# Kernel optimization log

Hardware: AMD Instinct MI355X
Metric: run time of the kernel (lower is better)

## Reference

```python
import jax, jax.numpy as jnp
import numpy as np

HID = 128
N_NODES = 50000
N_REL = 500
N_EDGES = 625000
BN_EPS = 1e-5
LRELU_SLOPE = 0.01


def _xavier(key, shape):
    fan_in, fan_out = shape[1], shape[0]
    std = float(np.sqrt(2.0 / (fan_in + fan_out)))
    return jax.random.normal(key, shape, dtype=jnp.float32) * std


def setup_inputs() -> dict:
    key = jax.random.key(0)
    ks = jax.random.split(key, 16)
    x = jax.random.normal(ks[0], (N_NODES, HID), dtype=jnp.float32)
    r = jax.random.normal(ks[1], (N_REL, HID), dtype=jnp.float32)
    que_context = jax.random.normal(ks[2], (1, HID), dtype=jnp.float32)
    fin_que = jax.random.normal(ks[3], (1, 1, HID), dtype=jnp.float32)
    edge_index = jax.random.randint(ks[4], (2, N_EDGES), 0, N_NODES, dtype=jnp.int64)
    edge_attr = jax.random.randint(ks[5], (N_EDGES,), 0, N_REL, dtype=jnp.int64)
    return {
        "x": x, "r": r, "que_context": que_context, "fin_que": fin_que,
        "edge_index": edge_index, "edge_attr": edge_attr,
        # mess_comp: Linear(2*hid, hid) + Tanh
        "W_mess": _xavier(ks[6], (HID, 2 * HID)), "b_mess": jnp.zeros((HID,), jnp.float32),
        # mess_atten_trans: Linear(2*hid, hid) + LeakyReLU
        "W_matt": _xavier(ks[7], (HID, 2 * HID)), "b_matt": jnp.zeros((HID,), jnp.float32),
        "mess_atten_weight": _xavier(ks[8], (1, HID)),
        # x_atten_trans: Linear(2*hid, hid) + LeakyReLU
        "W_xatt": _xavier(ks[9], (HID, 2 * HID)), "b_xatt": jnp.zeros((HID,), jnp.float32),
        "x_atten_weight": _xavier(ks[10], (1, HID)),
        # BatchNorm1d(hid) affine params (training-mode batch stats are used)
        "bn_gamma": jnp.ones((HID,), jnp.float32), "bn_beta": jnp.zeros((HID,), jnp.float32),
    }


def reference(x, r, que_context, fin_que, edge_index, edge_attr,
              W_mess, b_mess, W_matt, b_matt, mess_atten_weight,
              W_xatt, b_xatt, x_atten_weight, bn_gamma, bn_beta):
    n_nodes = x.shape[0]
    # BatchNorm1d over relation embeddings (training-mode: batch statistics, biased var)
    mu = jnp.mean(r, axis=0)
    var = jnp.mean(jnp.square(r - mu), axis=0)
    r = (r - mu) * jax.lax.rsqrt(var + BN_EPS) * bn_gamma + bn_beta

    head_ents, tail_ents = edge_index[0], edge_index[1]
    head_embeds = x[head_ents]            # [E, H]
    rel_embeds = r[edge_attr]             # [E, H]

    # message computation: Linear(2H->H) + tanh
    mess_in = jnp.concatenate([head_embeds, rel_embeds], axis=1)  # [E, 2H]
    mess = jnp.tanh(mess_in @ W_mess.T + b_mess)                  # [E, H]

    # message attention logits
    qc = jnp.broadcast_to(que_context, (mess.shape[0], que_context.shape[1]))
    mc = jnp.concatenate([mess, qc], axis=1) @ W_matt.T + b_matt
    mc = jax.nn.leaky_relu(mc, LRELU_SLOPE)
    mess_coeffs = jnp.sum(mess_atten_weight * mc, axis=1)         # [E]

    # segment softmax over tail_ents
    seg_max = jax.ops.segment_max(mess_coeffs, tail_ents, num_segments=n_nodes)
    mess_coeffs = jnp.exp(mess_coeffs - seg_max[tail_ents])
    seg_sum = jax.ops.segment_sum(mess_coeffs, tail_ents, num_segments=n_nodes)
    mess_weights = mess_coeffs / (seg_sum[tail_ents] + 1e-16)

    # weighted scatter-sum aggregation
    sum_mess = jax.ops.segment_sum(mess * mess_weights[:, None], tail_ents,
                                   num_segments=n_nodes)          # [N, H]

    # gating attention between x and aggregated messages
    pair = jnp.stack([x, sum_mess], axis=1)                       # [N, 2, H]
    fq = jnp.broadcast_to(fin_que, (n_nodes, 2, fin_que.shape[2]))
    xc = jnp.concatenate([pair, fq], axis=2)                      # [N, 2, 2H]
    xc = jax.nn.leaky_relu(jnp.einsum('nkc,hc->nkh', xc, W_xatt) + b_xatt, LRELU_SLOPE)
    x_coeffs = jnp.sum(x_atten_weight[None] * xc, axis=2)         # [N, 2]
    x_weight = jax.nn.softmax(x_coeffs, axis=1)
    x_out = x_weight[:, 0:1] * x + x_weight[:, 1:2] * sum_mess
    # dropout is identity (eval / p=0)
    return x_out, r
```

## Files before the change

### kernel.cpp

```cpp
#include <hip/hip_runtime.h>
#include <hip/hip_bf16.h>

#define HID 128
#define NN 50000
#define NR 500
#define NE 625000
#define LRELU 0.01f
#define SCAN_BLOCKS 196

typedef __hip_bfloat16 bf16;
typedef __attribute__((ext_vector_type(8))) short short8;
typedef __attribute__((ext_vector_type(4))) float float4_;

__device__ __forceinline__ float b2f(bf16 v) { return __bfloat162float(v); }
__device__ __forceinline__ bf16 f2b(float v) { return __float2bfloat16(v); }

__device__ __forceinline__ float san(float v) {
    return (v == v && v > -1e30f && v < 1e30f) ? v : 0.f;
}

__device__ __forceinline__ float ftanh(float a) {
    float e = __expf(2.f * a);
    return 1.f - 2.f * __builtin_amdgcn_rcpf(e + 1.f);
}

__device__ __forceinline__ float ldf(const void* p, int i, int f32) {
    return f32 ? ((const float*)p)[i] : b2f(((const bf16*)p)[i]);
}
__device__ __forceinline__ void stf(void* p, int i, float v, int f32) {
    if (f32) ((float*)p)[i] = v;
    else ((bf16*)p)[i] = f2b(v);
}

__device__ __forceinline__ int clampi(int v, int hi) {
    return v < 0 ? 0 : (v >= hi ? hi - 1 : v);
}
__device__ __forceinline__ int idx_at(const int* p, int i, int is64) {
    return p[is64 ? (2 * i) : i];
}

__device__ __forceinline__ unsigned short bfbits(float v) {
    bf16 h = f2b(v);
    return *(unsigned short*)&h;
}
__device__ __forceinline__ unsigned int packbf2(float a, float b) {
    return (unsigned int)bfbits(a) | ((unsigned int)bfbits(b) << 16);
}
__device__ __forceinline__ float bflo(unsigned int u) { return __uint_as_float(u << 16); }
__device__ __forceinline__ float bfhi(unsigned int u) { return __uint_as_float(u & 0xffff0000u); }

__device__ __forceinline__ float xorReduce16(float v) {
    v += __shfl_xor(v, 1, 64);
    v += __shfl_xor(v, 2, 64);
    v += __shfl_xor(v, 4, 64);
    v += __shfl_xor(v, 8, 64);
    return v;
}
__device__ __forceinline__ float waveMax(float v) {
#pragma unroll
    for (int o = 1; o < 64; o <<= 1) v = fmaxf(v, __shfl_xor(v, o, 64));
    return v;
}
__device__ __forceinline__ float waveSum(float v) {
#pragma unroll
    for (int o = 1; o < 64; o <<= 1) v += __shfl_xor(v, o, 64);
    return v;
}

struct DetectArr {
    const void* p[16];
    int sz[16];
    int kind[16];
};

__global__ void detect_all(DetectArr d, int* __restrict__ flags) {
    int b = blockIdx.x;
    if (d.kind[b] == 1) {
        if (threadIdx.x == 0) {
            const int* q = (const int*)d.p[b];
            int o = 0;
            for (int i = 0; i < 64; ++i) o |= q[2 * i + 1];
            flags[b] = (o == 0) ? 1 : 0;
        }
        return;
    }
    __shared__ int sb[64], sf[64];
    const unsigned int* w = (const unsigned int*)d.p[b];
    int K = d.sz[b] >> 1;
    if (K > 4096) K = 4096;
    int bv = 0, fv = 0;
    for (int i = threadIdx.x; i < K; i += 64) {
        unsigned int x = w[i];
        unsigned int lo = x & 0xFFFFu, hi = x >> 16;
        if (lo == 0u) {
            if (hi) fv++;
        } else {
            unsigned int e = (lo >> 7) & 0xFFu;
            if (e >= 90u && e <= 160u) bv++;
            else fv++;
        }
    }
    sb[threadIdx.x] = bv; sf[threadIdx.x] = fv;
    __syncthreads();
    if (threadIdx.x == 0) {
        int B = 0, F = 0;
        for (int i = 0; i < 64; ++i) { B += sb[i]; F += sf[i]; }
        flags[b] = (F > B) ? 1 : 0;
    }
}

__global__ void bn_stats(const void* __restrict__ r, const int* __restrict__ flags,
                         float* __restrict__ stats) {
    __shared__ float sb[256], sq[256];
    const int fr = flags[1];
    int h = blockIdx.x;
    int t = threadIdx.x;
    float s = 0.f, ss = 0.f;
    for (int i = t; i < NR; i += 256) {
        float v = ldf(r, i * HID + h, fr);
        s += v; ss += v * v;
    }
    sb[t] = s; sq[t] = ss;
    __syncthreads();
    for (int o = 128; o > 0; o >>= 1) {
        if (t < o) { sb[t] += sb[t + o]; sq[t] += sq[t + o]; }
        __syncthreads();
    }
    if (t == 0) {
        float mu = sb[0] / NR;
        float var = sq[0] / NR - mu * mu;
        if (var < 0.f) var = 0.f;
        stats[h] = mu;
        stats[HID + h] = rsqrtf(var + 1e-5f);
    }
}

__global__ void bn_apply(const void* __restrict__ r, const void* __restrict__ gamma,
                         const void* __restrict__ beta, const int* __restrict__ flags,
                         const float* __restrict__ stats,
                         float* __restrict__ rnorm, void* __restrict__ out_base) {
    const int fr = flags[1], fg = flags[14], fb = flags[15], fo = flags[0];
    int i = blockIdx.x * 256 + threadIdx.x;
    if (i >= NR * HID) return;
    int h = i & 127;
    float v = san((ldf(r, i, fr) - stats[h]) * stats[HID + h] * ldf(gamma, h, fg)
                  + ldf(beta, h, fb));
    rnorm[i] = v;
    stf(out_base, NN * HID + i, v, fo);
}

__global__ void precomp_kernel(const void* __restrict__ Wmatt, const void* __restrict__ bmatt,
                               const void* __restrict__ qc,
                               const void* __restrict__ Wxatt, const void* __restrict__ bxatt,
                               const void* __restrict__ fq, const int* __restrict__ flags,
                               float* __restrict__ cmatt, float* __restrict__ cxatt) {
    __shared__ float qcs[HID], fqs[HID];
    const int fWm = flags[8], fbm = flags[9], fqc = flags[2];
    const int fWx = flags[11], fbx = flags[12], ffq = flags[3];
    int h = threadIdx.x;
    qcs[h] = ldf(qc, h, fqc);
    fqs[h] = ldf(fq, h, ffq);
    __syncthreads();
    float a = ldf(bmatt, h, fbm), b = ldf(bxatt, h, fbx);
    for (int k = 0; k < HID; ++k) {
        a += ldf(Wmatt, h * 2 * HID + HID + k, fWm) * qcs[k];
        b += ldf(Wxatt, h * 2 * HID + HID + k, fWx) * fqs[k];
    }
    cmatt[h] = san(a);
    cxatt[h] = san(b);
}

__global__ void rm_kernel(const void* __restrict__ Wmess, const void* __restrict__ bmess,
                          const int* __restrict__ flags,
                          const float* __restrict__ rnorm, bf16* __restrict__ Rmb) {
    __shared__ float rl[HID];
    const int fW = flags[6], fb = flags[7];
    int rel = blockIdx.x, h = threadIdx.x;
    rl[h] = rnorm[rel * HID + h];
    __syncthreads();
    float a = ldf(bmess, h, fb);
    for (int k = 0; k < HID; ++k)
        a += ldf(Wmess, h * 2 * HID + HID + k, fW) * rl[k];
    Rmb[rel * HID + h] = f2b(san(a));
}

#define MLDA 136

__device__ __forceinline__ short8 load_bfrag(const void* W, int n, int k0, int f32) {
    short8 b;
    if (f32) {
        const float* Wf = (const float*)W + (size_t)n * 2 * HID + k0;
        float4 u0 = *(const float4*)Wf;
        float4 u1 = *(const float4*)(Wf + 4);
        b[0] = (short)bfbits(u0.x); b[1] = (short)bfbits(u0.y);
        b[2] = (short)bfbits(u0.z); b[3] = (short)bfbits(u0.w);
        b[4] = (short)bfbits(u1.x); b[5] = (short)bfbits(u1.y);
        b[6] = (short)bfbits(u1.z); b[7] = (short)bfbits(u1.w);
    } else {
        b = *(const short8*)((const bf16*)W + (size_t)n * 2 * HID + k0);
    }
    return b;
}

__global__ __launch_bounds__(256, 4) void xm_mfma(const void* __restrict__ x,
                                                  const void* __restrict__ Wmess,
                                                  const int* __restrict__ flags,
                                                  bf16* __restrict__ Xmb) {
    __shared__ short ml[64 * MLDA];
    const int fx = flags[0], fW = flags[6];
    int tid = threadIdx.x;
    int l = tid & 63, w = tid >> 6;
    int quad = l >> 4, lo16 = l & 15;
    int nbase = w * 32;
    short8 bfr[2][4];
#pragma unroll
    for (int nt = 0; nt < 2; ++nt)
#pragma unroll
        for (int kk = 0; kk < 4; ++kk)
            bfr[nt][kk] = load_bfrag(Wmess, nbase + nt * 16 + lo16, kk * 32 + quad * 8, fW);

    const int ntiles = (NN + 63) / 64;
    for (int tile = blockIdx.x; tile < ntiles; tile += gridDim.x) {
        __syncthreads();
#pragma unroll
        for (int p = 0; p < 8; ++p) {
            int rl_ = p * 8 + (tid >> 5);
            int node = clampi(tile * 64 + rl_, NN);
            int k4 = (tid & 31) * 4;
            unsigned int o0, o1;
            if (fx) {
                float4 v = *(const float4*)((const float*)x + (size_t)node * HID + k4);
                o0 = packbf2(v.x, v.y);
                o1 = packbf2(v.z, v.w);
            } else {
                uint2 u = *(const uint2*)((const bf16*)x + (size_t)node * HID + k4);
                o0 = u.x; o1 = u.y;
            }
            unsigned int* dst = (unsigned int*)&ml[rl_ * MLDA + k4];
            dst[0] = o0; dst[1] = o1;
        }
        __syncthreads();
        float4_ acc[4][2];
#pragma unroll
        for (int mt = 0; mt < 4; ++mt)
#pragma unroll
            for (int nt = 0; nt < 2; ++nt)
                acc[mt][nt] = (float4_){0.f, 0.f, 0.f, 0.f};
#pragma unroll
        for (int kk = 0; kk < 4; ++kk) {
            short8 a[4];
#pragma unroll
            for (int mt = 0; mt < 4; ++mt)
                a[mt] = *(const short8*)&ml[(mt * 16 + lo16) * MLDA + kk * 32 + quad * 8];
#pragma unroll
            for (int mt = 0; mt < 4; ++mt)
#pragma unroll
                for (int nt = 0; nt < 2; ++nt)
                    acc[mt][nt] = __builtin_amdgcn_mfma_f32_16x16x32_bf16(
                        a[mt], bfr[nt][kk], acc[mt][nt], 0, 0, 0);
        }
#pragma unroll
        for (int mt = 0; mt < 4; ++mt)
#pragma unroll
            for (int nt = 0; nt < 2; ++nt)
#pragma unroll
                for (int r = 0; r < 4; ++r) {
                    int node = tile * 64 + mt * 16 + quad * 4 + r;
                    if (node < NN)
                        Xmb[node * HID + nbase + nt * 16 + lo16] = f2b(san(acc[mt][nt][r]));
                }
    }
}

__global__ __launch_bounds__(256, 6) void edge_coeff_mfma(
        const bf16* __restrict__ Xmb, const bf16* __restrict__ Rmb,
        const void* __restrict__ Wmatt, const float* __restrict__ cmatt,
        const void* __restrict__ maw, const unsigned int* __restrict__ hrcsr,
        const int* __restrict__ flags, float* __restrict__ ccsr) {
    __shared__ short ml[64 * MLDA];
    __shared__ float swave[4][64];
    const int fWm = flags[8], fmw = flags[10];
    int tid = threadIdx.x;
    int l = tid & 63, w = tid >> 6;
    int quad = l >> 4, lo16 = l & 15;
    int nbase = w * 32;
    short8 bfr[2][4];
#pragma unroll
    for (int nt = 0; nt < 2; ++nt)
#pragma unroll
        for (int kk = 0; kk < 4; ++kk)
            bfr[nt][kk] = load_bfrag(Wmatt, nbase + nt * 16 + lo16, kk * 32 + quad * 8, fWm);

    int n0 = nbase + lo16, n1 = n0 + 16;
    float c0 = cmatt[n0], c1 = cmatt[n1];
    float w0 = ldf(maw, n0, fmw), w1 = ldf(maw, n1, fmw);

    const int ntiles = (NE + 63) / 64;
    const int seg = tid & 15;
    const int rowsub = tid >> 4;
    for (int T = blockIdx.x; T < ntiles; T += gridDim.x) {
        __syncthreads();
#pragma unroll
        for (int p = 0; p < 4; ++p) {
            int el = p * 16 + rowsub;
            int slot = T * 64 + el;
            unsigned int hr = hrcsr[slot < NE ? slot : NE - 1];
            int head = hr & 0xffffu, rel = hr >> 16;
            int k8 = seg * 8;
            uint4 xv = *(const uint4*)&Xmb[head * HID + k8];
            uint4 rv = *(const uint4*)&Rmb[rel * HID + k8];
            uint4 o;
            o.x = packbf2(ftanh(bflo(xv.x) + bflo(rv.x)), ftanh(bfhi(xv.x) + bfhi(rv.x)));
            o.y = packbf2(ftanh(bflo(xv.y) + bflo(rv.y)), ftanh(bfhi(xv.y) + bfhi(rv.y)));
            o.z = packbf2(ftanh(bflo(xv.z) + bflo(rv.z)), ftanh(bfhi(xv.z) + bfhi(rv.z)));
            o.w = packbf2(ftanh(bflo(xv.w) + bflo(rv.w)), ftanh(bfhi(xv.w) + bfhi(rv.w)));
            *(uint4*)&ml[el * MLDA + k8] = o;
        }
        __syncthreads();
        float4_ acc[4][2];
#pragma unroll
        for (int mt = 0; mt < 4; ++mt)
#pragma unroll
            for (int nt = 0; nt < 2; ++nt)
                acc[mt][nt] = (float4_){0.f, 0.f, 0.f, 0.f};
#pragma unroll
        for (int kk = 0; kk < 4; ++kk) {
            short8 a[4];
#pragma unroll
            for (int mt = 0; mt < 4; ++mt)
                a[mt] = *(const short8*)&ml[(mt * 16 + lo16) * MLDA + kk * 32 + quad * 8];
#pragma unroll
            for (int mt = 0; mt < 4; ++mt)
#pragma unroll
                for (int nt = 0; nt < 2; ++nt)
                    acc[mt][nt] = __builtin_amdgcn_mfma_f32_16x16x32_bf16(
                        a[mt], bfr[nt][kk], acc[mt][nt], 0, 0, 0);
        }
#pragma unroll
        for (int mt = 0; mt < 4; ++mt)
#pragma unroll
            for (int r = 0; r < 4; ++r) {
                float z0 = acc[mt][0][r] + c0;
                z0 = z0 > 0.f ? z0 : LRELU * z0;
                float z1 = acc[mt][1][r] + c1;
                z1 = z1 > 0.f ? z1 : LRELU * z1;
                float s = w0 * z0 + w1 * z1;
                s = xorReduce16(s);
                if (lo16 == 0) swave[w][mt * 16 + quad * 4 + r] = s;
            }
        __syncthreads();
        if (tid < 64) {
            int slot = T * 64 + tid;
            if (slot < NE)
                ccsr[slot] = san(swave[0][tid] + swave[1][tid] + swave[2][tid] + swave[3][tid]);
        }
    }
}

__global__ __launch_bounds__(256, 4) void gate_mfma(
        const void* __restrict__ x, const bf16* __restrict__ smb,
        const void* __restrict__ Wxatt, const float* __restrict__ cxatt,
        const void* __restrict__ xaw, const int* __restrict__ flags,
        void* __restrict__ outx) {
    __shared__ short ml[64 * MLDA];
    __shared__ float swave[4][64];
    __shared__ float lgL[64];
    const int fx = flags[0], fWx = flags[11], fxw = flags[13], fo = flags[0];
    int tid = threadIdx.x;
    int l = tid & 63, w = tid >> 6;
    int quad = l >> 4, lo16 = l & 15;
    int nbase = w * 32;
    short8 bfr[2][4];
#pragma unroll
    for (int nt = 0; nt < 2; ++nt)
#pragma unroll
        for (int kk = 0; kk < 4; ++kk)
            bfr[nt][kk] = load_bfrag(Wxatt, nbase + nt * 16 + lo16, kk * 32 + quad * 8, fWx);

    int n0 = nbase + lo16, n1 = n0 + 16;
    float c0 = cxatt[n0], c1 = cxatt[n1];
    float w0 = ldf(xaw, n0, fxw), w1 = ldf(xaw, n1, fxw);

    const int ntiles = (NN + 31) / 32;
    for (int tile = blockIdx.x; tile < ntiles; tile += gridDim.x) {
        __syncthreads();
#pragma unroll
        for (int p = 0; p < 8; ++p) {
            int rl_ = p * 8 + (tid >> 5);
            int node = clampi(tile * 32 + (rl_ >> 1), NN);
            int k4 = (tid & 31) * 4;
            unsigned int o0, o1;
            if (rl_ & 1) {
                uint2 u = *(const uint2*)&smb[node * HID + k4];
                o0 = u.x; o1 = u.y;
            } else if (fx) {
                float4 v = *(const float4*)((const float*)x + (size_t)node * HID + k4);
                o0 = packbf2(v.x, v.y);
                o1 = packbf2(v.z, v.w);
            } else {
                uint2 u = *(const uint2*)((const bf16*)x + (size_t)node * HID + k4);
                o0 = u.x; o1 = u.y;
            }
            unsigned int* dst = (unsigned int*)&ml[rl_ * MLDA + k4];
            dst[0] = o0; dst[1] = o1;
        }
        __syncthreads();
        float4_ acc[4][2];
#pragma unroll
        for (int mt = 0; mt < 4; ++mt)
#pragma unroll
            for (int nt = 0; nt < 2; ++nt)
                acc[mt][nt] = (float4_){0.f, 0.f, 0.f, 0.f};
#pragma unroll
        for (int kk = 0; kk < 4; ++kk) {
            short8 a[4];
#pragma unroll
            for (int mt = 0; mt < 4; ++mt)
                a[mt] = *(const short8*)&ml[(mt * 16 + lo16) * MLDA + kk * 32 + quad * 8];
#pragma unroll
            for (int mt = 0; mt < 4; ++mt)
#pragma unroll
                for (int nt = 0; nt < 2; ++nt)
                    acc[mt][nt] = __builtin_amdgcn_mfma_f32_16x16x32_bf16(
                        a[mt], bfr[nt][kk], acc[mt][nt], 0, 0, 0);
        }
#pragma unroll
        for (int mt = 0; mt < 4; ++mt)
#pragma unroll
            for (int r = 0; r < 4; ++r) {
                float z0 = acc[mt][0][r] + c0;
                z0 = z0 > 0.f ? z0 : LRELU * z0;
                float z1 = acc[mt][1][r] + c1;
                z1 = z1 > 0.f ? z1 : LRELU * z1;
                float s = w0 * z0 + w1 * z1;
                s = xorReduce16(s);
                if (lo16 == 0) swave[w][mt * 16 + quad * 4 + r] = s;
            }
        __syncthreads();
        if (tid < 64)
            lgL[tid] = san(swave[0][tid] + swave[1][tid] + swave[2][tid] + swave[3][tid]);
        __syncthreads();
#pragma unroll
        for (int it = 0; it < 16; ++it) {
            int idx = tid + 256 * it;
            int nl = idx >> 7, h = idx & 127;
            int node = tile * 32 + nl;
            if (node < NN) {
                float g0 = lgL[2 * nl], g1 = lgL[2 * nl + 1];
                float mm = fmaxf(g0, g1);
                float e0 = __expf(g0 - mm), e1 = __expf(g1 - mm);
                float inv = __builtin_amdgcn_rcpf(e0 + e1);
                float xv = ldf(x, node * HID + h, fx);
                float sv = b2f(smb[node * HID + h]);
                stf(outx, node * HID + h, san((e0 * xv + e1 * sv) * inv), fo);
            }
        }
    }
}

__global__ void count_kernel(const int* __restrict__ ei, const int* __restrict__ flags,
                             int* __restrict__ counts) {
    const int is64e = flags[4];
    for (int e = blockIdx.x * blockDim.x + threadIdx.x; e < NE; e += gridDim.x * blockDim.x) {
        int tail = clampi(idx_at(ei, NE + e, is64e), NN);
        atomicAdd(&counts[tail], 1);
    }
}

__global__ void scan_phase1(const int* __restrict__ counts, int* __restrict__ offs,
                            int* __restrict__ bsum) {
    __shared__ int buf[256];
    int t = threadIdx.x;
    int i = blockIdx.x * 256 + t;
    int v = (i < NN) ? counts[i] : 0;
    buf[t] = v;
    __syncthreads();
    for (int off = 1; off < 256; off <<= 1) {
        int add = (t >= off) ? buf[t - off] : 0;
        __syncthreads();
        buf[t] += add;
        __syncthreads();
    }
    if (i < NN) offs[i] = buf[t] - v;
    if (t == 255) bsum[blockIdx.x] = buf[255];
}

__global__ void scan_phase2(int* __restrict__ bsum, int* __restrict__ bexc) {
    __shared__ int buf[256];
    int t = threadIdx.x;
    int v = (t < SCAN_BLOCKS) ? bsum[t] : 0;
    buf[t] = v;
    __syncthreads();
    for (int off = 1; off < 256; off <<= 1) {
        int add = (t >= off) ? buf[t - off] : 0;
        __syncthreads();
        buf[t] += add;
        __syncthreads();
    }
    if (t < SCAN_BLOCKS) bexc[t] = buf[t] - v;
    if (t == 255) bexc[SCAN_BLOCKS] = buf[255];
}

__global__ void scan_phase3(int* __restrict__ offs, int* __restrict__ cursor,
                            const int* __restrict__ bexc) {
    int i = blockIdx.x * 256 + threadIdx.x;
    if (i < NN) {
        int v = offs[i] + bexc[blockIdx.x];
        offs[i] = v;
        cursor[i] = v;
    }
    if (i == 0) offs[NN] = bexc[SCAN_BLOCKS];
}

__global__ void scatter_kernel(const int* __restrict__ ei, const int* __restrict__ ea,
                               const int* __restrict__ flags,
                               int* __restrict__ cursor, unsigned int* __restrict__ hrcsr) {
    const int is64e = flags[4], is64a = flags[5];
    for (int e = blockIdx.x * blockDim.x + threadIdx.x; e < NE; e += gridDim.x * blockDim.x) {
        int tail = clampi(idx_at(ei, NE + e, is64e), NN);
        int head = clampi(idx_at(ei, e, is64e), NN);
        int rel = clampi(idx_at(ea, e, is64a), NR);
        int p = atomicAdd(&cursor[tail], 1);
        if (p >= 0 && p < NE)
            hrcsr[p] = (unsigned int)head | ((unsigned int)rel << 16);
    }
}

__global__ __launch_bounds__(256, 8) void node_aggr_kernel(
        const bf16* __restrict__ Xmb, const bf16* __restrict__ Rmb,
        const int* __restrict__ offs, const unsigned int* __restrict__ hrcsr,
        const float* __restrict__ ccsr, bf16* __restrict__ smb) {
    int tid = threadIdx.x;
    int sub = tid >> 6;
    int lane = tid & 63;
    int node = blockIdx.x * 4 + sub;
    if (node >= NN) return;
    int s = offs[node], en = offs[node + 1];

    float m = -INFINITY;
    for (int i = s + lane; i < en; i += 64) m = fmaxf(m, ccsr[i]);
    m = waveMax(m);
    float lsum = 0.f;
    for (int i = s + lane; i < en; i += 64) lsum += __expf(ccsr[i] - m);
    lsum = waveSum(lsum);
    float inv = 1.f / (lsum + 1e-16f);

    const int col = lane * 2;
    float acc0 = 0.f, acc1 = 0.f;
    int i = s;
    for (; i + 2 <= en; i += 2) {
        unsigned int hr0 = hrcsr[i], hr1 = hrcsr[i + 1];
        float wg0 = __expf(ccsr[i] - m), wg1 = __expf(ccsr[i + 1] - m);
        unsigned int xv0 = *(const unsigned int*)&Xmb[(hr0 & 0xffffu) * HID + col];
        unsigned int rv0 = *(const unsigned int*)&Rmb[(hr0 >> 16) * HID + col];
        unsigned int xv1 = *(const unsigned int*)&Xmb[(hr1 & 0xffffu) * HID + col];
        unsigned int rv1 = *(const unsigned int*)&Rmb[(hr1 >> 16) * HID + col];
        acc0 += wg0 * ftanh(bflo(xv0) + bflo(rv0)) + wg1 * ftanh(bflo(xv1) + bflo(rv1));
        acc1 += wg0 * ftanh(bfhi(xv0) + bfhi(rv0)) + wg1 * ftanh(bfhi(xv1) + bfhi(rv1));
    }
    if (i < en) {
        unsigned int hr0 = hrcsr[i];
        float wg0 = __expf(ccsr[i] - m);
        unsigned int xv0 = *(const unsigned int*)&Xmb[(hr0 & 0xffffu) * HID + col];
        unsigned int rv0 = *(const unsigned int*)&Rmb[(hr0 >> 16) * HID + col];
        acc0 += wg0 * ftanh(bflo(xv0) + bflo(rv0));
        acc1 += wg0 * ftanh(bfhi(xv0) + bfhi(rv0));
    }
    *(unsigned int*)&smb[node * HID + col] = packbf2(san(acc0 * inv), san(acc1 * inv));
}

extern "C" void kernel_launch(void* const* d_in, const int* in_sizes, int n_in,
                              void* d_out, int out_size, void* d_ws, size_t ws_size,
                              hipStream_t stream) {
    const void* x     = d_in[0];
    const void* r     = d_in[1];
    const void* qc    = d_in[2];
    const void* fq    = d_in[3];
    const int*  ei    = (const int*)d_in[4];
    const int*  ea    = (const int*)d_in[5];
    const void* Wmess = d_in[6];
    const void* bmess = d_in[7];
    const void* Wmatt = d_in[8];
    const void* bmatt = d_in[9];
    const void* maw   = d_in[10];
    const void* Wxatt = d_in[11];
    const void* bxatt = d_in[12];
    const void* xaw   = d_in[13];
    const void* gamma = d_in[14];
    const void* beta  = d_in[15];

    int*          flags  = (int*)d_ws;
    int*          counts = flags + 16;
    int*          offs   = counts + NN;
    int*          cursor = offs + NN + 1;
    int*          bsum   = cursor + NN + 3;
    int*          bexc   = bsum + 256;
    unsigned int* hrcsr  = (unsigned int*)(bexc + 260);
    float*        ccsr   = (float*)(hrcsr + NE);
    float*        rnorm  = ccsr + NE;
    float*        stats  = rnorm + (size_t)NR * HID;
    float*        cmatt  = stats + 2 * HID;
    float*        cxatt  = cmatt + HID;
    bf16*         Rmb    = (bf16*)(cxatt + HID);
    bf16*         Xmb    = Rmb + (size_t)NR * HID;
    bf16*         smb    = Xmb + (size_t)NN * HID;

    hipMemsetAsync(counts, 0, NN * sizeof(int), stream);

    DetectArr da;
    const void* ps[16] = {x, r, qc, fq, ei, ea, Wmess, bmess, Wmatt, bmatt, maw,
                          Wxatt, bxatt, xaw, gamma, beta};
    int szs[16] = {NN * HID, NR * HID, HID, HID, 2 * NE, NE, 2 * HID * HID, HID,
                   2 * HID * HID, HID, HID, 2 * HID * HID, HID, HID, HID, HID};
    for (int i = 0; i < 16; ++i) {
        da.p[i] = ps[i];
        da.sz[i] = szs[i];
        da.kind[i] = (i == 4 || i == 5) ? 1 : 0;
    }
    detect_all<<<16, 64, 0, stream>>>(da, flags);

    bn_stats<<<HID, 256, 0, stream>>>(r, flags, stats);
    bn_apply<<<(NR * HID + 255) / 256, 256, 0, stream>>>(r, gamma, beta, flags, stats,
                                                         rnorm, d_out);
    precomp_kernel<<<1, HID, 0, stream>>>(Wmatt, bmatt, qc, Wxatt, bxatt, fq, flags,
                                          cmatt, cxatt);
    rm_kernel<<<NR, HID, 0, stream>>>(Wmess, bmess, flags, rnorm, Rmb);
    xm_mfma<<<512, 256, 0, stream>>>(x, Wmess, flags, Xmb);
    count_kernel<<<1024, 256, 0, stream>>>(ei, flags, counts);
    scan_phase1<<<SCAN_BLOCKS, 256, 0, stream>>>(counts, offs, bsum);
    scan_phase2<<<1, 256, 0, stream>>>(bsum, bexc);
    scan_phase3<<<SCAN_BLOCKS, 256, 0, stream>>>(offs, cursor, bexc);
    scatter_kernel<<<1024, 256, 0, stream>>>(ei, ea, flags, cursor, hrcsr);
    edge_coeff_mfma<<<1536, 256, 0, stream>>>(Xmb, Rmb, Wmatt, cmatt, maw, hrcsr, flags,
                                              ccsr);
    node_aggr_kernel<<<(NN + 3) / 4, 256, 0, stream>>>(Xmb, Rmb, offs, hrcsr, ccsr, smb);
    gate_mfma<<<512, 256, 0, stream>>>(x, smb, Wxatt, cxatt, xaw, flags, d_out);
}
```

Baseline: 445.7 us.

## Fuse edge attention scoring with segment softmax and aggregation in node-aligned tiles

```diff
diff --git a/kernel.cpp b/kernel.cpp
--- a/kernel.cpp
+++ b/kernel.cpp
@@ -7,6 +7,7 @@
 #define NE 625000
 #define LRELU 0.01f
 #define SCAN_BLOCKS 196
+#define NT_TILES ((NE + 63) / 64)
 
 typedef __hip_bfloat16 bf16;
 typedef __attribute__((ext_vector_type(8))) short short8;
@@ -54,16 +55,6 @@
     v += __shfl_xor(v, 2, 64);
     v += __shfl_xor(v, 4, 64);
     v += __shfl_xor(v, 8, 64);
-    return v;
-}
-__device__ __forceinline__ float waveMax(float v) {
-#pragma unroll
-    for (int o = 1; o < 64; o <<= 1) v = fmaxf(v, __shfl_xor(v, o, 64));
-    return v;
-}
-__device__ __forceinline__ float waveSum(float v) {
-#pragma unroll
-    for (int o = 1; o < 64; o <<= 1) v += __shfl_xor(v, o, 64);
     return v;
 }
 
@@ -272,13 +263,29 @@
     }
 }
 
-__global__ __launch_bounds__(256, 6) void edge_coeff_mfma(
+__global__ void build_tiles(const int* __restrict__ offs, int* __restrict__ tns) {
+    int t = blockIdx.x * 256 + threadIdx.x;
+    if (t > NT_TILES) return;
+    int target = t * 64;
+    int lo = 0, hi = NN;
+    while (lo < hi) {
+        int mid = (lo + hi) >> 1;
+        if (offs[mid] >= target) hi = mid; else lo = mid + 1;
+    }
+    tns[t] = lo;
+}
+
+__global__ __launch_bounds__(256, 4) void edge_fused_mfma(
         const bf16* __restrict__ Xmb, const bf16* __restrict__ Rmb,
         const void* __restrict__ Wmatt, const float* __restrict__ cmatt,
-        const void* __restrict__ maw, const unsigned int* __restrict__ hrcsr,
-        const int* __restrict__ flags, float* __restrict__ ccsr) {
-    __shared__ short ml[64 * MLDA];
+        const void* __restrict__ maw, const int* __restrict__ offs,
+        const unsigned int* __restrict__ hrcsr, const int* __restrict__ tns,
+        const int* __restrict__ flags, bf16* __restrict__ smb) {
+    __shared__ short ml[128 * MLDA];
     __shared__ float swave[4][64];
+    __shared__ float lg[128];
+    __shared__ float wgt[128];
+    __shared__ int shdr[4];
     const int fWm = flags[8], fmw = flags[10];
     int tid = threadIdx.x;
     int l = tid & 63, w = tid >> 6;
@@ -295,16 +302,26 @@
     float c0 = cmatt[n0], c1 = cmatt[n1];
     float w0 = ldf(maw, n0, fmw), w1 = ldf(maw, n1, fmw);
 
-    const int ntiles = (NE + 63) / 64;
     const int seg = tid & 15;
     const int rowsub = tid >> 4;
-    for (int T = blockIdx.x; T < ntiles; T += gridDim.x) {
-        __syncthreads();
-#pragma unroll
-        for (int p = 0; p < 4; ++p) {
-            int el = p * 16 + rowsub;
-            int slot = T * 64 + el;
-            unsigned int hr = hrcsr[slot < NE ? slot : NE - 1];
+
+    for (int T = blockIdx.x; T < NT_TILES; T += gridDim.x) {
+        __syncthreads();
+        if (tid == 0) {
+            int a = tns[T], b = tns[T + 1];
+            shdr[0] = a; shdr[1] = b;
+            shdr[2] = offs[a];
+            shdr[3] = offs[b];
+        }
+        __syncthreads();
+        int nodeS = shdr[0], nodeE = shdr[1];
+        if (nodeE <= nodeS) continue;
+        int slot0 = shdr[2];
+        int count = shdr[3] - slot0;
+        if (count > 128) count = 128;
+
+        for (int el = rowsub; el < count; el += 16) {
+            unsigned int hr = hrcsr[slot0 + el];
             int head = hr & 0xffffu, rel = hr >> 16;
             int k8 = seg * 8;
             uint4 xv = *(const uint4*)&Xmb[head * HID + k8];
@@ -317,42 +334,79 @@
             *(uint4*)&ml[el * MLDA + k8] = o;
         }
         __syncthreads();
-        float4_ acc[4][2];
-#pragma unroll
-        for (int mt = 0; mt < 4; ++mt)
-#pragma unroll
-            for (int nt = 0; nt < 2; ++nt)
-                acc[mt][nt] = (float4_){0.f, 0.f, 0.f, 0.f};
-#pragma unroll
-        for (int kk = 0; kk < 4; ++kk) {
-            short8 a[4];
+
+        int npass = (count + 63) >> 6;
+        for (int pass = 0; pass < npass; ++pass) {
+            float4_ acc[4][2];
 #pragma unroll
             for (int mt = 0; mt < 4; ++mt)
-                a[mt] = *(const short8*)&ml[(mt * 16 + lo16) * MLDA + kk * 32 + quad * 8];
+#pragma unroll
+                for (int nt = 0; nt < 2; ++nt)
+                    acc[mt][nt] = (float4_){0.f, 0.f, 0.f, 0.f};
+#pragma unroll
+            for (int kk = 0; kk < 4; ++kk) {
+                short8 a[4];
+#pragma unroll
+                for (int mt = 0; mt < 4; ++mt)
+                    a[mt] = *(const short8*)&ml[(pass * 64 + mt * 16 + lo16) * MLDA
+                                                + kk * 32 + quad * 8];
+#pragma unroll
+                for (int mt = 0; mt < 4; ++mt)
+#pragma unroll
+                    for (int nt = 0; nt < 2; ++nt)
+                        acc[mt][nt] = __builtin_amdgcn_mfma_f32_16x16x32_bf16(
+                            a[mt], bfr[nt][kk], acc[mt][nt], 0, 0, 0);
+            }
 #pragma unroll
             for (int mt = 0; mt < 4; ++mt)
 #pragma unroll
-                for (int nt = 0; nt < 2; ++nt)
-                    acc[mt][nt] = __builtin_amdgcn_mfma_f32_16x16x32_bf16(
-                        a[mt], bfr[nt][kk], acc[mt][nt], 0, 0, 0);
-        }
-#pragma unroll
-        for (int mt = 0; mt < 4; ++mt)
-#pragma unroll
-            for (int r = 0; r < 4; ++r) {
-                float z0 = acc[mt][0][r] + c0;
-                z0 = z0 > 0.f ? z0 : LRELU * z0;
-                float z1 = acc[mt][1][r] + c1;
-                z1 = z1 > 0.f ? z1 : LRELU * z1;
-                float s = w0 * z0 + w1 * z1;
-                s = xorReduce16(s);
-                if (lo16 == 0) swave[w][mt * 16 + quad * 4 + r] = s;
+                for (int r = 0; r < 4; ++r) {
+                    float z0 = acc[mt][0][r] + c0;
+                    z0 = z0 > 0.f ? z0 : LRELU * z0;
+                    float z1 = acc[mt][1][r] + c1;
+                    z1 = z1 > 0.f ? z1 : LRELU * z1;
+                    float s = w0 * z0 + w1 * z1;
+                    s = xorReduce16(s);
+                    if (lo16 == 0) swave[w][mt * 16 + quad * 4 + r] = s;
+                }
+            __syncthreads();
+            if (tid < 64)
+                lg[pass * 64 + tid] = san(swave[0][tid] + swave[1][tid]
+                                          + swave[2][tid] + swave[3][tid]);
+            __syncthreads();
+        }
+
+        for (int n = nodeS + tid; n < nodeE; n += 256) {
+            int s = offs[n] - slot0;
+            int e = offs[n + 1] - slot0;
+            if (s > 128) s = 128;
+            if (e > 128) e = 128;
+            float m = -INFINITY;
+            for (int i = s; i < e; ++i) m = fmaxf(m, lg[i]);
+            float sum = 0.f;
+            for (int i = s; i < e; ++i) {
+                float ev = __expf(lg[i] - m);
+                wgt[i] = ev;
+                sum += ev;
             }
-        __syncthreads();
-        if (tid < 64) {
-            int slot = T * 64 + tid;
-            if (slot < NE)
-                ccsr[slot] = san(swave[0][tid] + swave[1][tid] + swave[2][tid] + swave[3][tid]);
+            float inv = 1.f / (sum + 1e-16f);
+            for (int i = s; i < e; ++i) wgt[i] *= inv;
+        }
+        __syncthreads();
+
+        for (int n = nodeS + w; n < nodeE; n += 4) {
+            int s = offs[n] - slot0;
+            int e = offs[n + 1] - slot0;
+            if (s > 128) s = 128;
+            if (e > 128) e = 128;
+            float acc0 = 0.f, acc1 = 0.f;
+            for (int i = s; i < e; ++i) {
+                float wv = wgt[i];
+                unsigned int u = *(const unsigned int*)&ml[i * MLDA + l * 2];
+                acc0 += wv * bflo(u);
+                acc1 += wv * bfhi(u);
+            }
+            *(unsigned int*)&smb[n * HID + 2 * l] = packbf2(san(acc0), san(acc1));
         }
     }
 }
@@ -524,49 +578,6 @@
         if (p >= 0 && p < NE)
             hrcsr[p] = (unsigned int)head | ((unsigned int)rel << 16);
     }
-}
-
-__global__ __launch_bounds__(256, 8) void node_aggr_kernel(
-        const bf16* __restrict__ Xmb, const bf16* __restrict__ Rmb,
-        const int* __restrict__ offs, const unsigned int* __restrict__ hrcsr,
-        const float* __restrict__ ccsr, bf16* __restrict__ smb) {
-    int tid = threadIdx.x;
-    int sub = tid >> 6;
-    int lane = tid & 63;
-    int node = blockIdx.x * 4 + sub;
-    if (node >= NN) return;
-    int s = offs[node], en = offs[node + 1];
-
-    float m = -INFINITY;
-    for (int i = s + lane; i < en; i += 64) m = fmaxf(m, ccsr[i]);
-    m = waveMax(m);
-    float lsum = 0.f;
-    for (int i = s + lane; i < en; i += 64) lsum += __expf(ccsr[i] - m);
-    lsum = waveSum(lsum);
-    float inv = 1.f / (lsum + 1e-16f);
-
-    const int col = lane * 2;
-    float acc0 = 0.f, acc1 = 0.f;
-    int i = s;
-    for (; i + 2 <= en; i += 2) {
-        unsigned int hr0 = hrcsr[i], hr1 = hrcsr[i + 1];
-        float wg0 = __expf(ccsr[i] - m), wg1 = __expf(ccsr[i + 1] - m);
-        unsigned int xv0 = *(const unsigned int*)&Xmb[(hr0 & 0xffffu) * HID + col];
-        unsigned int rv0 = *(const unsigned int*)&Rmb[(hr0 >> 16) * HID + col];
-        unsigned int xv1 = *(const unsigned int*)&Xmb[(hr1 & 0xffffu) * HID + col];
-        unsigned int rv1 = *(const unsigned int*)&Rmb[(hr1 >> 16) * HID + col];
-        acc0 += wg0 * ftanh(bflo(xv0) + bflo(rv0)) + wg1 * ftanh(bflo(xv1) + bflo(rv1));
-        acc1 += wg0 * ftanh(bfhi(xv0) + bfhi(rv0)) + wg1 * ftanh(bfhi(xv1) + bfhi(rv1));
-    }
-    if (i < en) {
-        unsigned int hr0 = hrcsr[i];
-        float wg0 = __expf(ccsr[i] - m);
-        unsigned int xv0 = *(const unsigned int*)&Xmb[(hr0 & 0xffffu) * HID + col];
-        unsigned int rv0 = *(const unsigned int*)&Rmb[(hr0 >> 16) * HID + col];
-        acc0 += wg0 * ftanh(bflo(xv0) + bflo(rv0));
-        acc1 += wg0 * ftanh(bfhi(xv0) + bfhi(rv0));
-    }
-    *(unsigned int*)&smb[node * HID + col] = packbf2(san(acc0 * inv), san(acc1 * inv));
 }
 
 extern "C" void kernel_launch(void* const* d_in, const int* in_sizes, int n_in,
@@ -596,8 +607,8 @@
     int*          bsum   = cursor + NN + 3;
     int*          bexc   = bsum + 256;
     unsigned int* hrcsr  = (unsigned int*)(bexc + 260);
-    float*        ccsr   = (float*)(hrcsr + NE);
-    float*        rnorm  = ccsr + NE;
+    int*          tns    = (int*)(hrcsr + NE);
+    float*        rnorm  = (float*)(tns + NE);
     float*        stats  = rnorm + (size_t)NR * HID;
     float*        cmatt  = stats + 2 * HID;
     float*        cxatt  = cmatt + HID;
@@ -630,9 +641,9 @@
     scan_phase1<<<SCAN_BLOCKS, 256, 0, stream>>>(counts, offs, bsum);
     scan_phase2<<<1, 256, 0, stream>>>(bsum, bexc);
     scan_phase3<<<SCAN_BLOCKS, 256, 0, stream>>>(offs, cursor, bexc);
+    build_tiles<<<(NT_TILES + 256) / 256, 256, 0, stream>>>(offs, tns);
     scatter_kernel<<<1024, 256, 0, stream>>>(ei, ea, flags, cursor, hrcsr);
-    edge_coeff_mfma<<<1536, 256, 0, stream>>>(Xmb, Rmb, Wmatt, cmatt, maw, hrcsr, flags,
-                                              ccsr);
-    node_aggr_kernel<<<(NN + 3) / 4, 256, 0, stream>>>(Xmb, Rmb, offs, hrcsr, ccsr, smb);
+    edge_fused_mfma<<<1536, 256, 0, stream>>>(Xmb, Rmb, Wmatt, cmatt, maw, offs, hrcsr,
+                                              tns, flags, smb);
     gate_mfma<<<512, 256, 0, stream>>>(x, smb, Wxatt, cxatt, xaw, flags, d_out);
 }
```

After: 517.5 us. +16.1%, slower.
